# Kernel tuning notes

Hardware: AMD Instinct MI355X
Metric: run time of the kernel (lower is better)

Reference implementation:

```python
import jax, jax.numpy as jnp
import numpy as np

NUM_LAYERS = 3
NUM_NODES = 120000  # num_users + num_items
LATENT_DIM = 64
NUM_EDGES = 2000000


def setup_inputs() -> dict:
    key = jax.random.key(0)
    k1, k2 = jax.random.split(key)
    edge_index = jax.random.randint(k1, (2, NUM_EDGES), 0, NUM_NODES, dtype=jnp.int64 if jax.config.jax_enable_x64 else jnp.int32)
    # init_parameters: normal(std=0.1) for LightGCN
    emb_weight = jax.random.normal(k2, (NUM_NODES, LATENT_DIM), dtype=jnp.float32) * 0.1
    return {"edge_index": edge_index, "emb_weight": emb_weight}


def reference(edge_index, emb_weight):
    """RecSysGNN (model='LightGCN') forward. Returns (emb0, out)."""
    n = emb_weight.shape[0]
    src, dst = edge_index[0], edge_index[1]
    # degree of target nodes (degree(to_, x.size(0)))
    deg = jax.ops.segment_sum(jnp.ones(src.shape[0], dtype=emb_weight.dtype), dst, num_segments=n)
    deg_inv_sqrt = jnp.where(deg > 0, jax.lax.rsqrt(jnp.maximum(deg, 1.0)), 0.0)
    norm = deg_inv_sqrt[src] * deg_inv_sqrt[dst]  # [E]

    emb0 = emb_weight
    emb = emb0
    acc = emb0  # running sum of layer embeddings for final mean
    for _ in range(NUM_LAYERS):
        msg = norm[:, None] * emb[src]                      # [E, d] gather + scale
        emb = jax.ops.segment_sum(msg, dst, num_segments=n)  # scatter-add to targets
        acc = acc + emb
    out = acc / (NUM_LAYERS + 1)  # mean over stacked [emb0, emb1, ..., embL]
    return (emb0, out)
```

## Files before the change

### kernel.cpp

```cpp
#include <hip/hip_runtime.h>


#define DIM 64
#define BN 512
#define BSH 9
#define CHUNK 4096

typedef unsigned short u16;
typedef unsigned int u32;

static __device__ __forceinline__ float bf2f_lo(u32 p) { return __uint_as_float(p << 16); }
static __device__ __forceinline__ float bf2f_hi(u32 p) { return __uint_as_float(p & 0xffff0000u); }
static __device__ __forceinline__ u16 f2bf(float f) {
    unsigned u = __float_as_uint(f);
    return (u16)((u + 0x7fffu + ((u >> 16) & 1u)) >> 16);
}
static __device__ __forceinline__ u32 pack2(float a, float b) {
    return (u32)f2bf(a) | ((u32)f2bf(b) << 16);
}

__global__ void zero_cur(int* __restrict__ cursor) { cursor[threadIdx.x] = 0; }

__global__ void __launch_bounds__(512) c1_scatter(
        const int* __restrict__ src, const int* __restrict__ dst,
        int* __restrict__ cursor, u32* __restrict__ slab, int E, int CAP) {
    __shared__ u32 buf[CHUNK];
    __shared__ unsigned char bb[CHUNK];
    __shared__ int posb[256], startb[256], gbase[256];
    int w = blockIdx.x, tid = threadIdx.x;
    int lo = w * CHUNK, hi = min(lo + CHUNK, E);
    if (tid < 256) posb[tid] = 0;
    __syncthreads();
    for (int i = lo + tid; i < hi; i += 512) atomicAdd(&posb[dst[i] >> BSH], 1);
    __syncthreads();
    int x = 0;
    if (tid < 256) {
        x = posb[tid];
        gbase[tid] = x ? atomicAdd(cursor + tid, x) : 0;
    }
    __syncthreads();
    for (int off = 1; off < 256; off <<= 1) {
        int t = (tid >= off && tid < 256) ? posb[tid - off] : 0;
        __syncthreads();
        if (tid < 256) posb[tid] += t;
        __syncthreads();
    }
    if (tid < 256) startb[tid] = posb[tid] - x;
    __syncthreads();
    if (tid < 256) posb[tid] = startb[tid];
    __syncthreads();
    for (int i = lo + tid; i < hi; i += 512) {
        int d = dst[i], b = d >> BSH;
        int q = atomicAdd(&posb[b], 1);
        buf[q] = ((u32)src[i] << BSH) | (u32)(d & (BN - 1));
        bb[q] = (unsigned char)b;
    }
    __syncthreads();
    int n = hi - lo;
    for (int q = tid; q < n; q += 512) {
        int b = bb[q];
        slab[(size_t)b * CAP + gbase[b] + (q - startb[b])] = buf[q];
    }
}

__global__ void __launch_bounds__(512) c3_build(
        const u32* __restrict__ slab, const int* __restrict__ cursor,
        int* __restrict__ col, int2* __restrict__ row_se, float* __restrict__ dis,
        int N, int CAP, int NB) {
    __shared__ int cur[BN];
    __shared__ int ps[512];
    int b = blockIdx.x, tid = threadIdx.x;
    int xc = (tid < NB) ? cursor[tid] : 0;
    if (tid < 256) ps[tid] = xc;
    __syncthreads();
    for (int off = 1; off < 256; off <<= 1) {
        int t = (tid >= off && tid < 256) ? ps[tid - off] : 0;
        __syncthreads();
        if (tid < 256) ps[tid] += t;
        __syncthreads();
    }
    int lo  = b ? ps[b - 1] : 0;
    int cnt = cursor[b];
    __syncthreads();

    int nodeBase = b << BSH;
    int nLoc = min(BN, N - nodeBase);
    const u32* sp = slab + (size_t)b * CAP;
    cur[tid] = 0;
    __syncthreads();
    for (int i = tid; i < cnt; i += 512) atomicAdd(&cur[sp[i] & (BN - 1)], 1);
    __syncthreads();
    int c0 = cur[tid];
    ps[tid] = c0;
    __syncthreads();
    for (int off = 1; off < 512; off <<= 1) {
        int t = (tid >= off) ? ps[tid - off] : 0;
        __syncthreads();
        ps[tid] += t;
        __syncthreads();
    }
    int base = ps[tid] - c0;
    cur[tid] = base;
    if (tid < nLoc) {
        dis[nodeBase + tid] = c0 ? rsqrtf((float)c0) : 0.f;
        row_se[nodeBase + tid] = make_int2(lo + base, lo + base + c0);
    }
    __syncthreads();
    for (int i = tid; i < cnt; i += 512) {
        u32 v = sp[i];
        int q = atomicAdd(&cur[v & (BN - 1)], 1);
        col[lo + q] = (int)(v >> BSH);
    }
}

__global__ void cvt_copy(const float4* __restrict__ emb, const float* __restrict__ dis,
                         ushort4* __restrict__ e0b, float4* __restrict__ emb0_out, int n4) {
    int i = blockIdx.x * blockDim.x + threadIdx.x;
    if (i < n4) {
        float4 v = emb[i];
        float w = dis[i >> 4];
        ushort4 o;
        o.x = f2bf(w * v.x); o.y = f2bf(w * v.y);
        o.z = f2bf(w * v.z); o.w = f2bf(w * v.w);
        e0b[i] = o;
        emb0_out[i] = v;
    }
}

#define GATHER_BODY(CURTAB)                                                    \
    float sx = 0.f, sy = 0.f;                                                  \
    int j = start;                                                             \
    for (; j + 16 <= end; j += 16) {                                           \
        int jj = j + half;                                                     \
        _Pragma("unroll")                                                      \
        for (int k = 0; k < 8; ++k) {                                          \
            u32 p = (CURTAB)[col[jj + 2 * k] * 32 + d2];                       \
            sx += bf2f_lo(p);                                                  \
            sy += bf2f_hi(p);                                                  \
        }                                                                      \
    }                                                                          \
    if (j < end) {                                                             \
        int endm1 = end - 1;                                                   \
        int jj = j + half;                                                     \
        _Pragma("unroll")                                                      \
        for (int k = 0; k < 8; ++k) {                                          \
            int e  = jj + 2 * k;                                               \
            u32 p  = (CURTAB)[col[min(e, endm1)] * 32 + d2];                   \
            if (e >= end) p = 0;                                               \
            sx += bf2f_lo(p);                                                  \
            sy += bf2f_hi(p);                                                  \
        }                                                                      \
    }                                                                          \
    sx += __shfl_xor(sx, 32);                                                  \
    sy += __shfl_xor(sy, 32);

__global__ void __launch_bounds__(256) gather_mid(
        const int2* __restrict__ row_se, const int* __restrict__ col,
        const float* __restrict__ dis, const u32* __restrict__ cur,
        u32* __restrict__ next, int N) {
    int t = blockIdx.x * blockDim.x + threadIdx.x;
    int wave = t >> 6, lane = t & 63;
    if (wave >= N) return;
    int half = lane >> 5, d2 = lane & 31;
    int2 se = row_se[wave];
    int start = __builtin_amdgcn_readfirstlane(se.x);
    int end   = __builtin_amdgcn_readfirstlane(se.y);
    GATHER_BODY(cur)
    float w = dis[wave];
    if (half == 0) next[wave * 32 + d2] = pack2(w * w * sx, w * w * sy);
}

__global__ void __launch_bounds__(256) gather_final(
        const int2* __restrict__ row_se, const int* __restrict__ col,
        const float* __restrict__ dis, const u32* __restrict__ cur ,
        const u32* __restrict__ e1b, const float2* __restrict__ emb0,
        float2* __restrict__ out, int N) {
    int t = blockIdx.x * blockDim.x + threadIdx.x;
    int wave = t >> 6, lane = t & 63;
    if (wave >= N) return;
    int half = lane >> 5, d2 = lane & 31;
    int2 se = row_se[wave];
    int start = __builtin_amdgcn_readfirstlane(se.x);
    int end   = __builtin_amdgcn_readfirstlane(se.y);
    GATHER_BODY(cur)
    if (half == 0) {
        float w = dis[wave];
        float inv = (w > 0.f) ? 1.0f / w : 0.f;
        float ex = w * sx, ey = w * sy;
        int idx = wave * 32 + d2;
        u32 q1 = e1b[idx], q2 = cur[idx];
        float2 e0 = emb0[idx];
        float ox = 0.25f * (e0.x + (bf2f_lo(q1) + bf2f_lo(q2)) * inv + ex);
        float oy = 0.25f * (e0.y + (bf2f_hi(q1) + bf2f_hi(q2)) * inv + ey);
        out[idx] = make_float2(ox, oy);
    }
}

extern "C" void kernel_launch(void* const* d_in, const int* in_sizes, int n_in,
                              void* d_out, int out_size, void* d_ws, size_t ws_size,
                              hipStream_t stream) {
    const int*   edge  = (const int*)d_in[0];
    const float* emb_w = (const float*)d_in[1];
    const int E = in_sizes[0] / 2;
    const int N = in_sizes[1] / DIM;
    const int* src = edge;
    const int* dst = edge + E;

    const int NB  = (N + BN - 1) >> BSH;
    const int nCh = (E + CHUNK - 1) / CHUNK;
    const int CAP = (E / (NB > 0 ? NB : 1)) * 2;

    float* out_base = (float*)d_out;
    float* emb0_out = out_base;
    float* acc      = out_base + (size_t)N * DIM;

    float* dis       = (float*)d_ws;
    int2*  row_se    = (int2*)(dis + ((N + 1) & ~1));
    int*   cursor    = (int*)(row_se + N);
    int*   col       = cursor + 256;
    u32*   slab      = (u32*)(col + E);
    u16*   e0b       = (u16*)slab;
    u16*   e1b       = e0b + (size_t)N * DIM;

    const int n4  = N * DIM / 4;
    const int BLK = 256;
    const int g4  = (n4 + BLK - 1) / BLK;
    const int gW  = (N * DIM + BLK - 1) / BLK;

    zero_cur<<<1, 256, 0, stream>>>(cursor);
    c1_scatter<<<nCh, 512, 0, stream>>>(src, dst, cursor, slab, E, CAP);
    c3_build<<<NB, 512, 0, stream>>>(slab, cursor, col, row_se, dis, N, CAP, NB);

    cvt_copy<<<g4, BLK, 0, stream>>>((const float4*)emb_w, dis,
                                     (ushort4*)e0b, (float4*)emb0_out, n4);

    gather_mid<<<gW, BLK, 0, stream>>>(row_se, col, dis, (const u32*)e0b, (u32*)e1b, N);
    gather_mid<<<gW, BLK, 0, stream>>>(row_se, col, dis, (const u32*)e1b, (u32*)e0b, N);
    gather_final<<<gW, BLK, 0, stream>>>(row_se, col, dis, (const u32*)e0b, (const u32*)e1b,
                                         (const float2*)emb_w, (float2*)acc, N);
}
```

Baseline: 280.5 us.

## Process two nodes per wavefront with 8-byte vectorized bf16 row gathers

Each wavefront now handles two destination nodes, one per 32-lane half. Within a half, two 16-lane groups split the edges, and each lane loads a uint2 (four bf16 values) instead of a single u32. This halves the grid size, raises bytes per load instruction and removes the idle half-wave writes. The cost is that the edge loop bounds are no longer wave-uniform: the two nodes in a wave have different degrees, so the wave diverges and runs as long as the busier node.

```diff
diff --git a/kernel.cpp b/kernel.cpp
--- a/kernel.cpp
+++ b/kernel.cpp
@@ -128,71 +128,83 @@
 }
 
 #define GATHER_BODY(CURTAB)                                                    \
-    float sx = 0.f, sy = 0.f;                                                  \
-    int j = start;                                                             \
-    for (; j + 16 <= end; j += 16) {                                           \
-        int jj = j + half;                                                     \
-        _Pragma("unroll")                                                      \
-        for (int k = 0; k < 8; ++k) {                                          \
-            u32 p = (CURTAB)[col[jj + 2 * k] * 32 + d2];                       \
-            sx += bf2f_lo(p);                                                  \
-            sy += bf2f_hi(p);                                                  \
+    float s0 = 0.f, s1 = 0.f, s2 = 0.f, s3 = 0.f;                              \
+    {                                                                          \
+        int j = start;                                                         \
+        for (; j + 8 <= end; j += 8) {                                         \
+            _Pragma("unroll")                                                  \
+            for (int k = 0; k < 4; ++k) {                                      \
+                int c = col[j + 2 * k + g];                                    \
+                uint2 p = *(const uint2*)((CURTAB) + (((size_t)c) << 5) + 2 * d); \
+                s0 += bf2f_lo(p.x); s1 += bf2f_hi(p.x);                        \
+                s2 += bf2f_lo(p.y); s3 += bf2f_hi(p.y);                        \
+            }                                                                  \
+        }                                                                      \
+        if (j < end) {                                                         \
+            int endm1 = end - 1;                                               \
+            _Pragma("unroll")                                                  \
+            for (int k = 0; k < 4; ++k) {                                      \
+                int e = j + 2 * k + g;                                         \
+                int c = col[min(e, endm1)];                                    \
+                uint2 p = *(const uint2*)((CURTAB) + (((size_t)c) << 5) + 2 * d); \
+                if (e >= end) { p.x = 0; p.y = 0; }                            \
+                s0 += bf2f_lo(p.x); s1 += bf2f_hi(p.x);                        \
+                s2 += bf2f_lo(p.y); s3 += bf2f_hi(p.y);                        \
+            }                                                                  \
         }                                                                      \
     }                                                                          \
-    if (j < end) {                                                             \
-        int endm1 = end - 1;                                                   \
-        int jj = j + half;                                                     \
-        _Pragma("unroll")                                                      \
-        for (int k = 0; k < 8; ++k) {                                          \
-            int e  = jj + 2 * k;                                               \
-            u32 p  = (CURTAB)[col[min(e, endm1)] * 32 + d2];                   \
-            if (e >= end) p = 0;                                               \
-            sx += bf2f_lo(p);                                                  \
-            sy += bf2f_hi(p);                                                  \
-        }                                                                      \
-    }                                                                          \
-    sx += __shfl_xor(sx, 32);                                                  \
-    sy += __shfl_xor(sy, 32);
+    s0 += __shfl_xor(s0, 16); s1 += __shfl_xor(s1, 16);                        \
+    s2 += __shfl_xor(s2, 16); s3 += __shfl_xor(s3, 16);
 
 __global__ void __launch_bounds__(256) gather_mid(
         const int2* __restrict__ row_se, const int* __restrict__ col,
         const float* __restrict__ dis, const u32* __restrict__ cur,
         u32* __restrict__ next, int N) {
     int t = blockIdx.x * blockDim.x + threadIdx.x;
-    int wave = t >> 6, lane = t & 63;
-    if (wave >= N) return;
-    int half = lane >> 5, d2 = lane & 31;
-    int2 se = row_se[wave];
-    int start = __builtin_amdgcn_readfirstlane(se.x);
-    int end   = __builtin_amdgcn_readfirstlane(se.y);
+    int pair = t >> 6, lane = t & 63;
+    if (2 * pair >= N) return;
+    int node = 2 * pair + (lane >> 5);
+    int g = (lane >> 4) & 1, d = lane & 15;
+    bool valid = node < N;
+    int2 se = valid ? row_se[node] : make_int2(0, 0);
+    int start = se.x, end = se.y;
     GATHER_BODY(cur)
-    float w = dis[wave];
-    if (half == 0) next[wave * 32 + d2] = pack2(w * w * sx, w * w * sy);
+    if (valid && g == 0) {
+        float w = dis[node], ww = w * w;
+        uint2 o;
+        o.x = pack2(ww * s0, ww * s1);
+        o.y = pack2(ww * s2, ww * s3);
+        *(uint2*)(next + (((size_t)node) << 5) + 2 * d) = o;
+    }
 }
 
 __global__ void __launch_bounds__(256) gather_final(
         const int2* __restrict__ row_se, const int* __restrict__ col,
         const float* __restrict__ dis, const u32* __restrict__ cur ,
-        const u32* __restrict__ e1b, const float2* __restrict__ emb0,
-        float2* __restrict__ out, int N) {
+        const u32* __restrict__ e1b, const float* __restrict__ emb0,
+        float* __restrict__ out, int N) {
     int t = blockIdx.x * blockDim.x + threadIdx.x;
-    int wave = t >> 6, lane = t & 63;
-    if (wave >= N) return;
-    int half = lane >> 5, d2 = lane & 31;
-    int2 se = row_se[wave];
-    int start = __builtin_amdgcn_readfirstlane(se.x);
-    int end   = __builtin_amdgcn_readfirstlane(se.y);
+    int pair = t >> 6, lane = t & 63;
+    if (2 * pair >= N) return;
+    int node = 2 * pair + (lane >> 5);
+    int g = (lane >> 4) & 1, d = lane & 15;
+    bool valid = node < N;
+    int2 se = valid ? row_se[node] : make_int2(0, 0);
+    int start = se.x, end = se.y;
     GATHER_BODY(cur)
-    if (half == 0) {
-        float w = dis[wave];
+    if (valid && g == 0) {
+        float w = dis[node];
         float inv = (w > 0.f) ? 1.0f / w : 0.f;
-        float ex = w * sx, ey = w * sy;
-        int idx = wave * 32 + d2;
-        u32 q1 = e1b[idx], q2 = cur[idx];
-        float2 e0 = emb0[idx];
-        float ox = 0.25f * (e0.x + (bf2f_lo(q1) + bf2f_lo(q2)) * inv + ex);
-        float oy = 0.25f * (e0.y + (bf2f_hi(q1) + bf2f_hi(q2)) * inv + ey);
-        out[idx] = make_float2(ox, oy);
+        size_t idx = (((size_t)node) << 5) + 2 * d;
+        uint2 q1 = *(const uint2*)(e1b + idx);
+        uint2 q2 = *(const uint2*)(cur + idx);
+        float4 e0 = *(const float4*)(emb0 + 2 * idx);
+        float4 r;
+        r.x = 0.25f * (e0.x + (bf2f_lo(q1.x) + bf2f_lo(q2.x)) * inv + w * s0);
+        r.y = 0.25f * (e0.y + (bf2f_hi(q1.x) + bf2f_hi(q2.x)) * inv + w * s1);
+        r.z = 0.25f * (e0.z + (bf2f_lo(q1.y) + bf2f_lo(q2.y)) * inv + w * s2);
+        r.w = 0.25f * (e0.w + (bf2f_hi(q1.y) + bf2f_hi(q2.y)) * inv + w * s3);
+        *(float4*)(out + 2 * idx) = r;
     }
 }
 
@@ -222,10 +234,11 @@
     u16*   e0b       = (u16*)slab;
     u16*   e1b       = e0b + (size_t)N * DIM;
 
-    const int n4  = N * DIM / 4;
-    const int BLK = 256;
-    const int g4  = (n4 + BLK - 1) / BLK;
-    const int gW  = (N * DIM + BLK - 1) / BLK;
+    const int n4    = N * DIM / 4;
+    const int BLK   = 256;
+    const int g4    = (n4 + BLK - 1) / BLK;
+    const int PAIRS = (N + 1) / 2;
+    const int gW    = (PAIRS * 64 + BLK - 1) / BLK;
 
     zero_cur<<<1, 256, 0, stream>>>(cursor);
     c1_scatter<<<nCh, 512, 0, stream>>>(src, dst, cursor, slab, E, CAP);
@@ -237,5 +250,5 @@
     gather_mid<<<gW, BLK, 0, stream>>>(row_se, col, dis, (const u32*)e0b, (u32*)e1b, N);
     gather_mid<<<gW, BLK, 0, stream>>>(row_se, col, dis, (const u32*)e1b, (u32*)e0b, N);
     gather_final<<<gW, BLK, 0, stream>>>(row_se, col, dis, (const u32*)e0b, (const u32*)e1b,
-                                         (const float2*)emb_w, (float2*)acc, N);
-}
+                                         emb_w, acc, N);
+}
```

Measured after the change: 262.5 us. 1.07x faster.
